# Performance work log

Measured on AMD Instinct MI355X. Metric: run time of the kernel, lower is better.

The kernel has to match this reference:

```python
import jax, jax.numpy as jnp
import numpy as np

B, T, E, H = 4, 2048, 1024, 16
D = E // H

def setup_inputs() -> dict:
    key = jax.random.key(0)
    ks = jax.random.split(key, 8)
    s = 0.02
    return {
        "q": jax.random.normal(ks[0], (B, T, E), dtype=jnp.float32),
        "k": jax.random.normal(ks[1], (B, T, E), dtype=jnp.float32),
        "v": jax.random.normal(ks[2], (B, T, E), dtype=jnp.float32),
        "Wq": jax.random.normal(ks[3], (E, E), dtype=jnp.float32) * s,
        "Wk": jax.random.normal(ks[4], (E, E), dtype=jnp.float32) * s,
        "Wv": jax.random.normal(ks[5], (E, E), dtype=jnp.float32) * s,
        "Wp": jax.random.normal(ks[6], (E, E), dtype=jnp.float32) * s,
        "bp": jnp.zeros((E,), dtype=jnp.float32),
    }

def reference(q, k, v, Wq, Wk, Wv, Wp, bp):
    # Linear projections (torch Linear: x @ W.T). NOTE: original code computes
    # key from the already-projected query (k = self.key(q)); external k is unused.
    qp = q @ Wq.T                      # [B,T,E]
    kp = qp @ Wk.T                     # [B,T,E]  <- faithful quirk
    vp = v @ Wv.T                      # [B,T,E]
    qh = qp.reshape(B, T, H, D).transpose(0, 2, 1, 3)  # [B,H,T,D]
    kh = kp.reshape(B, T, H, D).transpose(0, 2, 1, 3)
    vh = vp.reshape(B, T, H, D).transpose(0, 2, 1, 3)
    # Faithful quirk: att = scores / D**(-1/2) == scores * sqrt(D)
    scale = jnp.float32(D) ** 0.5
    att = jnp.einsum('bhtd,bhsd->bhts', qh, kh) * scale  # [B,H,T,T]
    causal = jnp.tril(jnp.ones((T, T), dtype=bool))
    att = jnp.where(causal, att, -jnp.inf)
    att = jax.nn.softmax(att, axis=-1)
    y = jnp.einsum('bhts,bhsd->bhtd', att, vh)           # [B,H,T,D]
    y = y.transpose(0, 2, 1, 3).reshape(B, T, E)
    return y @ Wp.T + bp
```

## Files before the change

### kernel.cpp

```cpp
#include <hip/hip_runtime.h>


typedef unsigned short u16;
typedef unsigned int   u32;
typedef __attribute__((ext_vector_type(8))) __bf16 bf16x8;
typedef __attribute__((ext_vector_type(8))) u16    u16x8;
typedef __attribute__((ext_vector_type(4))) u16    u16x4;
typedef __attribute__((ext_vector_type(4))) float  f32x4;
typedef __attribute__((ext_vector_type(4))) int    i32x4;

#define DEV static __device__ __forceinline__

DEV u16 f2bf(float x){ union{float f;u32 u;}v; v.f=x; u32 r=v.u+0x7fffu+((v.u>>16)&1u); return (u16)(r>>16); }
DEV float bf2f(u16 b){ union{u32 u;float f;}v; v.u=((u32)b)<<16; return v.f; }
DEV f32x4 zero4(){ f32x4 z={0.f,0.f,0.f,0.f}; return z; }
DEV f32x4 mfma16(bf16x8 a, bf16x8 b, f32x4 c){ return __builtin_amdgcn_mfma_f32_16x16x32_bf16(a,b,c,0,0,0); }
DEV void gld16(const u16* g, u16* l){
  __builtin_amdgcn_global_load_lds((const __attribute__((address_space(1))) u32*)g,
                                   (__attribute__((address_space(3))) u32*)l, 16, 0, 0);
}
DEV u32 cvtpk(float lo, float hi){
  u32 r;
  asm("v_cvt_pk_bf16_f32 %0, %1, %2" : "=v"(r) : "v"(lo), "v"(hi));
  return r;
}

constexpr int B_=4, T_=2048, E_=1024;
constexpr int M_=B_*T_;
constexpr float L2E8 = 11.5415603f;

__global__ __launch_bounds__(256)
void cvt_a(const float* __restrict__ q, const float* __restrict__ v,
           u16* __restrict__ qi, u16* __restrict__ vb)
{
  const int j=blockIdx.y;
  const size_t e=((size_t)blockIdx.x*256+threadIdx.x)*8;
  const float* s=(j==0)?q:v;
  f32x4 x0=*reinterpret_cast<const f32x4*>(s+e);
  f32x4 x1=*reinterpret_cast<const f32x4*>(s+e+4);
  u16x8 h,l;
#pragma unroll
  for(int t=0;t<4;t++){
    u16 hh=f2bf(x0[t]); h[t]=hh; l[t]=f2bf(x0[t]-bf2f(hh));
    u16 h2=f2bf(x1[t]); h[t+4]=h2; l[t+4]=f2bf(x1[t]-bf2f(h2));
  }
  if(j==0){
    const size_t row=e>>10, k=e&1023;
    u16* d=qi + row*2048 + (k>>3)*16;
    *reinterpret_cast<u16x8*>(d)=h;
    *reinterpret_cast<u16x8*>(d+8)=l;
  } else {
    *reinterpret_cast<u16x8*>(vb+e)=h;
  }
}

__global__ __launch_bounds__(256)
void cvt_w(const float* __restrict__ Wq, const float* __restrict__ Wk, const float* __restrict__ Wv,
           u16* __restrict__ wqi, u16* __restrict__ wki, u16* __restrict__ wvb)
{
  const int j=blockIdx.y;
  const size_t e=((size_t)blockIdx.x*256+threadIdx.x)*8;
  const float* s=(j==0)?Wq:(j==1)?Wk:Wv;
  f32x4 x0=*reinterpret_cast<const f32x4*>(s+e);
  f32x4 x1=*reinterpret_cast<const f32x4*>(s+e+4);
  u16x8 h,l;
#pragma unroll
  for(int t=0;t<4;t++){
    u16 hh=f2bf(x0[t]); h[t]=hh; l[t]=f2bf(x0[t]-bf2f(hh));
    u16 h2=f2bf(x1[t]); h[t+4]=h2; l[t+4]=f2bf(x1[t]-bf2f(h2));
  }
  if(j==2){ *reinterpret_cast<u16x8*>(wvb+e)=h; return; }
  u16* base=(j==0)?wqi:wki;
  const size_t row=e>>10, k=e&1023;
  u16* d=base + row*2048 + (k>>3)*16;
  *reinterpret_cast<u16x8*>(d)=h;
  *reinterpret_cast<u16x8*>(d+8)=l;
}

__global__ __launch_bounds__(256)
void cvt_p(const float* __restrict__ Wp, u16* __restrict__ wpb)
{
  const size_t e=((size_t)blockIdx.x*256+threadIdx.x)*8;
  f32x4 x0=*reinterpret_cast<const f32x4*>(Wp+e);
  f32x4 x1=*reinterpret_cast<const f32x4*>(Wp+e+4);
  u16x8 h;
#pragma unroll
  for(int t=0;t<4;t++){ h[t]=f2bf(x0[t]); h[t+4]=f2bf(x1[t]); }
  *reinterpret_cast<u16x8*>(wpb+e)=h;
}

template<int SPLIT,int OMODE>
__global__ __launch_bounds__(256)
void gemm(const u16* __restrict__ Ag, const u16* __restrict__ Bg,
          const float* __restrict__ bias,
          u16* __restrict__ Ob, float* __restrict__ Of, int ldc)
{
  __shared__ u16 sA[SPLIT?128*128:128*64];
  __shared__ u16 sB[SPLIT?128*128:128*64];

  const int tid=threadIdx.x, wave=tid>>6, lane=tid&63;
  const int quad=lane>>4, l16=lane&15, sw=l16&7;
  const int wm=(wave>>1)*64, wn=(wave&1)*64;
  const int n0=blockIdx.x*128, m0=blockIdx.y*128;

  f32x4 acc[4][4];
#pragma unroll
  for(int i=0;i<4;i++)
#pragma unroll
    for(int j=0;j<4;j++) acc[i][j]=zero4();

  for(int k0=0;k0<E_;k0+=64){
    if(SPLIT){
#pragma unroll
      for(int it=0;it<8;it++){
        const int c=it*256+tid, row=c>>4, j=(c&15)^(row&7);
        gld16(Ag + (size_t)(m0+row)*2048 + k0*2 + j*8, &sA[(it*256+wave*64)*8]);
      }
#pragma unroll
      for(int it=0;it<8;it++){
        const int c=it*256+tid, row=c>>4, j=(c&15)^(row&7);
        gld16(Bg + (size_t)(n0+row)*2048 + k0*2 + j*8, &sB[(it*256+wave*64)*8]);
      }
    } else {
#pragma unroll
      for(int it=0;it<4;it++){
        const int c=it*256+tid, row=c>>3, j=(c&7)^(row&7);
        gld16(Ag + (size_t)(m0+row)*1024 + k0 + j*8, &sA[(it*256+wave*64)*8]);
      }
#pragma unroll
      for(int it=0;it<4;it++){
        const int c=it*256+tid, row=c>>3, j=(c&7)^(row&7);
        gld16(Bg + (size_t)(n0+row)*1024 + k0 + j*8, &sB[(it*256+wave*64)*8]);
      }
    }
    __syncthreads();

#pragma unroll
    for(int kk=0;kk<2;kk++){
      if(SPLIT){
        bf16x8 ahh[4],ahl[4],bhh[4],bhl[4];
#pragma unroll
        for(int i=0;i<4;i++){
          const u16* pa=&sA[(wm+i*16+l16)*128];
          const u16* pb=&sB[(wn+i*16+l16)*128];
          const int ch=2*(kk*4+quad);
          ahh[i]=*reinterpret_cast<const bf16x8*>(&pa[((ch  )^sw)*8]);
          ahl[i]=*reinterpret_cast<const bf16x8*>(&pa[((ch+1)^sw)*8]);
          bhh[i]=*reinterpret_cast<const bf16x8*>(&pb[((ch  )^sw)*8]);
          bhl[i]=*reinterpret_cast<const bf16x8*>(&pb[((ch+1)^sw)*8]);
        }
#pragma unroll
        for(int i=0;i<4;i++)
#pragma unroll
          for(int j=0;j<4;j++){
            acc[i][j]=mfma16(ahh[i],bhh[j],acc[i][j]);
            acc[i][j]=mfma16(ahh[i],bhl[j],acc[i][j]);
            acc[i][j]=mfma16(ahl[i],bhh[j],acc[i][j]);
          }
      } else {
        bf16x8 a[4],b[4];
#pragma unroll
        for(int i=0;i<4;i++){
          a[i]=*reinterpret_cast<const bf16x8*>(&sA[(wm+i*16+l16)*64 + (((kk*4+quad)^sw)*8)]);
          b[i]=*reinterpret_cast<const bf16x8*>(&sB[(wn+i*16+l16)*64 + (((kk*4+quad)^sw)*8)]);
        }
#pragma unroll
        for(int i=0;i<4;i++)
#pragma unroll
          for(int j=0;j<4;j++)
            acc[i][j]=mfma16(a[i],b[j],acc[i][j]);
      }
    }
    __syncthreads();
  }

#pragma unroll
  for(int i=0;i<4;i++)
#pragma unroll
    for(int j=0;j<4;j++){
      const int col=n0+wn+j*16+l16;
#pragma unroll
      for(int r=0;r<4;r++){
        const int row=m0+wm+i*16+quad*4+r;
        float v=acc[i][j][r];
        if(OMODE==2)      Of[(size_t)row*ldc+col]=v+bias[col];
        else if(OMODE==1) Ob[(size_t)row*ldc+col]=f2bf(v);
        else {
          u16 hh=f2bf(v);
          const size_t base=(size_t)row*2048 + (size_t)(col>>3)*16 + (col&7);
          Ob[base]=hh; Ob[base+8]=f2bf(v-bf2f(hh));
        }
      }
    }
}

__global__ __launch_bounds__(256)
void attn(const u16* __restrict__ qpi, const u16* __restrict__ kpi,
          const u16* __restrict__ vpT, u16* __restrict__ yout)
{
  __shared__ u16 sK [2][64*128];
  __shared__ u16 sVT[2][64*64];

  const int tid=threadIdx.x, wave=tid>>6, lane=tid&63;
  const int quad=lane>>4, l16=lane&15, sw=l16&7;
  const int pr=(int)blockIdx.x>>6;
  const int bh=blockIdx.x&63;
  const int b=bh>>4, h=bh&15;

  auto STAGE=[&](int buf, int kt2){
    const int s0=kt2*64;
#pragma unroll
    for(int it=0;it<4;it++){
      const int c=it*256+tid, row=c>>4, j=(c&15)^(row&7);
      gld16(kpi + (size_t)(b*T_+s0+row)*2048 + h*128 + j*8,
            &sK[buf][(it*256+wave*64)*8]);
    }
#pragma unroll
    for(int it=0;it<2;it++){
      const int c=it*256+tid, row=c>>3, j=(c&7)^(row&7);
      gld16(vpT + (size_t)(h*64+row)*8192 + b*T_ + s0 + j*8,
            &sVT[buf][(it*256+wave*64)*8]);
    }
  };

#pragma unroll 1
  for(int half=0; half<2; half++){
    const int qt = half ? (15-pr) : pr;
    const int qr0=qt*128+wave*32;

    bf16x8 qfh[2][2], qfl[2][2];
#pragma unroll
    for(int mt=0;mt<2;mt++)
#pragma unroll
      for(int ksv=0;ksv<2;ksv++){
        const size_t off=(size_t)(b*T_+qr0+mt*16+l16)*2048 + h*128 + (ksv*4+quad)*16;
        qfh[mt][ksv]=*reinterpret_cast<const bf16x8*>(qpi+off);
        qfl[mt][ksv]=*reinterpret_cast<const bf16x8*>(qpi+off+8);
      }

    float mst[2]={-1e30f,-1e30f}, lst[2]={0.f,0.f};
    f32x4 oacc[2][4];
#pragma unroll
    for(int mt=0;mt<2;mt++)
#pragma unroll
      for(int dt=0;dt<4;dt++) oacc[mt][dt]=zero4();

    const int nkt=2*(qt+1);
    STAGE(0, 0);
    __syncthreads();

    for(int kt=0;kt<nkt;kt++){
      const int cur=kt&1;
      if(kt+1<nkt) STAGE(cur^1, kt+1);
      const int s0=kt*64;

      if(s0<=qr0+31){
        f32x4 sacc[4][2];
#pragma unroll
        for(int st=0;st<4;st++)
#pragma unroll
          for(int mt=0;mt<2;mt++) sacc[st][mt]=zero4();
        __builtin_amdgcn_s_setprio(1);
#pragma unroll
        for(int st=0;st<4;st++)
#pragma unroll
          for(int ksv=0;ksv<2;ksv++){
            const u16* pk=&sK[cur][(st*16+l16)*128];
            const int ch=2*(ksv*4+quad);
            bf16x8 kh=*reinterpret_cast<const bf16x8*>(&pk[((ch  )^sw)*8]);
            bf16x8 kl=*reinterpret_cast<const bf16x8*>(&pk[((ch+1)^sw)*8]);
#pragma unroll
            for(int mt=0;mt<2;mt++){
              sacc[st][mt]=mfma16(kh,qfh[mt][ksv],sacc[st][mt]);
              sacc[st][mt]=mfma16(kl,qfh[mt][ksv],sacc[st][mt]);
              sacc[st][mt]=mfma16(kh,qfl[mt][ksv],sacc[st][mt]);
            }
          }
        __builtin_amdgcn_s_setprio(0);
        const bool needmask=(s0+63>qr0);
        u32 pk_[4][2][2];
#pragma unroll
        for(int mt=0;mt<2;mt++){
          const int qrow=qr0+mt*16+l16;
          float mloc=-1e30f;
#pragma unroll
          for(int st=0;st<4;st++)
#pragma unroll
            for(int r=0;r<4;r++){
              float v=sacc[st][mt][r];
              if(needmask && (s0+st*16+quad*4+r>qrow)) v=-1e30f;
              sacc[st][mt][r]=v;
              mloc=fmaxf(mloc,v);
            }
          mloc=fmaxf(mloc,__shfl_xor(mloc,16,64));
          mloc=fmaxf(mloc,__shfl_xor(mloc,32,64));
          float cexp;
          if(__all(mloc <= mst[mt]+1.0f)){
            cexp=mst[mt]*L2E8;
          } else {
            const float nm=fmaxf(mst[mt],mloc);
            const float alpha=exp2f((mst[mt]-nm)*L2E8);
            mst[mt]=nm;
            lst[mt]*=alpha;
#pragma unroll
            for(int dt=0;dt<4;dt++) oacc[mt][dt]*=alpha;
            cexp=nm*L2E8;
          }
          float rs=0.f;
#pragma unroll
          for(int st=0;st<4;st++)
#pragma unroll
            for(int r=0;r<4;r++){
              float p=exp2f(__builtin_fmaf(sacc[st][mt][r],L2E8,-cexp));
              sacc[st][mt][r]=p;
              rs+=p;
            }
          lst[mt]+=rs;
#pragma unroll
          for(int st=0;st<4;st++){
            pk_[st][mt][0]=cvtpk(sacc[st][mt][0],sacc[st][mt][1]);
            pk_[st][mt][1]=cvtpk(sacc[st][mt][2],sacc[st][mt][3]);
          }
        }
        const int srcA=(2*(quad&1))*16+l16, srcB=srcA+16;
        const bool hs=(quad>=2);
#pragma unroll
        for(int ksv=0;ksv<2;ksv++){
          bf16x8 b2[2];
#pragma unroll
          for(int mt=0;mt<2;mt++){
            int e0=__shfl((int)pk_[2*ksv  ][mt][0],srcA,64);
            int g0=__shfl((int)pk_[2*ksv+1][mt][0],srcA,64);
            int e1=__shfl((int)pk_[2*ksv  ][mt][1],srcA,64);
            int g1=__shfl((int)pk_[2*ksv+1][mt][1],srcA,64);
            int e2=__shfl((int)pk_[2*ksv  ][mt][0],srcB,64);
            int g2=__shfl((int)pk_[2*ksv+1][mt][0],srcB,64);
            int e3=__shfl((int)pk_[2*ksv  ][mt][1],srcB,64);
            int g3=__shfl((int)pk_[2*ksv+1][mt][1],srcB,64);
            i32x4 bd={ hs?g0:e0, hs?g1:e1, hs?g2:e2, hs?g3:e3 };
            b2[mt]=*reinterpret_cast<bf16x8*>(&bd);
          }
          __builtin_amdgcn_s_setprio(1);
#pragma unroll
          for(int dt=0;dt<4;dt++){
            bf16x8 va=*reinterpret_cast<const bf16x8*>(&sVT[cur][(dt*16+l16)*64 + (((ksv*4+quad)^sw)*8)]);
#pragma unroll
            for(int mt=0;mt<2;mt++)
              oacc[mt][dt]=mfma16(va,b2[mt],oacc[mt][dt]);
          }
          __builtin_amdgcn_s_setprio(0);
        }
      }
      __syncthreads();
    }

#pragma unroll
    for(int mt=0;mt<2;mt++){
      float lt=lst[mt];
      lt+=__shfl_xor(lt,16,64);
      lt+=__shfl_xor(lt,32,64);
      const float inv=1.0f/lt;
      const size_t rb=(size_t)(b*T_+qr0+mt*16+l16)*1024 + h*64;
#pragma unroll
      for(int dt=0;dt<4;dt++){
        u16x4 o4;
#pragma unroll
        for(int r=0;r<4;r++) o4[r]=f2bf(oacc[mt][dt][r]*inv);
        *reinterpret_cast<u16x4*>(yout + rb + dt*16 + quad*4)=o4;
      }
    }
  }
}

extern "C" void kernel_launch(void* const* d_in, const int* in_sizes, int n_in,
                              void* d_out, int out_size, void* d_ws, size_t ws_size,
                              hipStream_t stream)
{
  const float* q =(const float*)d_in[0];
  const float* v =(const float*)d_in[2];
  const float* Wq=(const float*)d_in[3];
  const float* Wk=(const float*)d_in[4];
  const float* Wv=(const float*)d_in[5];
  const float* Wp=(const float*)d_in[6];
  const float* bp=(const float*)d_in[7];
  float* out=(float*)d_out;

  const size_t NE=(size_t)M_*E_;
  const size_t WE=(size_t)E_*E_;
  u16* wsv=(u16*)d_ws;
  u16* qsl_i=wsv;
  u16* qp_i =wsv+2*NE;
  u16* kp_i =wsv;
  u16* wp_b =wsv+2*NE;
  u16* vpT  =wsv+4*NE;
  u16* ybf  =wsv+5*NE;
  u16* og   =(u16*)d_out;
  u16* wq_i =og;
  u16* wk_i =og+2*WE;
  u16* wv_b =og+4*WE;
  u16* vb   =og+5*WE;

  dim3 blk(256);
  cvt_a<<<dim3(NE/2048,2), blk, 0, stream>>>(q, v, qsl_i, vb);
  cvt_w<<<dim3(WE/2048,3), blk, 0, stream>>>(Wq, Wk, Wv, wq_i, wk_i, wv_b);

  dim3 g(E_/128, M_/128);
  gemm<1,0><<<g, blk, 0, stream>>>(qsl_i, wq_i, nullptr, qp_i, nullptr, 0);
  gemm<1,0><<<g, blk, 0, stream>>>(qp_i, wk_i, nullptr, kp_i, nullptr, 0);
  gemm<0,1><<<dim3(M_/128, E_/128), blk, 0, stream>>>(wv_b, vb, nullptr, vpT, nullptr, M_);
  attn<<<dim3(512), blk, 0, stream>>>(qp_i, kp_i, vpT, ybf);
  cvt_p<<<dim3(WE/2048), blk, 0, stream>>>(Wp, wp_b);
  gemm<0,2><<<g, blk, 0, stream>>>(ybf, wp_b, bp, nullptr, out, E_);
}
```

Baseline: 433.1 us.

## Split attention KV range across wave pairs with 512-thread blocks and merge

The attention kernel now launches 512 threads per block. Each pair of waves shares the same 32 query rows and splits each 128-key tile in half, one 64-key half per wave. Per-wave online-softmax states (max, sum, output accumulators) are merged through shared memory at the end. K staging moves to 128-row double buffers with a single V buffer and explicit vmcnt waits and barriers, aiming for more waves in flight and fewer loop iterations. The cost is more LDS, extra barriers per iteration and a merge step.

```diff
diff --git a/kernel.cpp b/kernel.cpp
--- a/kernel.cpp
+++ b/kernel.cpp
@@ -194,39 +194,42 @@
     }
 }
 
-__global__ __launch_bounds__(256)
+__global__ __launch_bounds__(512,4)
 void attn(const u16* __restrict__ qpi, const u16* __restrict__ kpi,
           const u16* __restrict__ vpT, u16* __restrict__ yout)
 {
-  __shared__ u16 sK [2][64*128];
-  __shared__ u16 sVT[2][64*64];
+  __shared__ u16 sK [2][128*128];
+  __shared__ u16 sVT[64*128];
 
   const int tid=threadIdx.x, wave=tid>>6, lane=tid&63;
   const int quad=lane>>4, l16=lane&15, sw=l16&7;
+  const int rg=wave>>1, rho=wave&1;
   const int pr=(int)blockIdx.x>>6;
   const int bh=blockIdx.x&63;
   const int b=bh>>4, h=bh&15;
 
-  auto STAGE=[&](int buf, int kt2){
-    const int s0=kt2*64;
+  auto STAGE_K=[&](int buf, int j2){
 #pragma unroll
     for(int it=0;it<4;it++){
-      const int c=it*256+tid, row=c>>4, j=(c&15)^(row&7);
-      gld16(kpi + (size_t)(b*T_+s0+row)*2048 + h*128 + j*8,
-            &sK[buf][(it*256+wave*64)*8]);
-    }
+      const int c=it*512+tid, row=c>>4, j=(c&15)^(row&7);
+      gld16(kpi + (size_t)(b*T_+j2*128+row)*2048 + h*128 + j*8,
+            &sK[buf][(it*512+wave*64)*8]);
+    }
+  };
+  auto STAGE_V=[&](int j2){
 #pragma unroll
     for(int it=0;it<2;it++){
-      const int c=it*256+tid, row=c>>3, j=(c&7)^(row&7);
-      gld16(vpT + (size_t)(h*64+row)*8192 + b*T_ + s0 + j*8,
-            &sVT[buf][(it*256+wave*64)*8]);
+      const int c=it*512+tid, row=c>>4, j=(c&15)^(row&7);
+      gld16(vpT + (size_t)(h*64+row)*8192 + b*T_ + j2*128 + j*8,
+            &sVT[(it*512+wave*64)*8]);
     }
   };
 
 #pragma unroll 1
   for(int half=0; half<2; half++){
     const int qt = half ? (15-pr) : pr;
-    const int qr0=qt*128+wave*32;
+    const int qr0=qt*128+rg*32;
+    const int np=qt+1;
 
     bf16x8 qfh[2][2], qfl[2][2];
 #pragma unroll
@@ -245,16 +248,24 @@
 #pragma unroll
       for(int dt=0;dt<4;dt++) oacc[mt][dt]=zero4();
 
-    const int nkt=2*(qt+1);
-    STAGE(0, 0);
-    __syncthreads();
-
-    for(int kt=0;kt<nkt;kt++){
-      const int cur=kt&1;
-      if(kt+1<nkt) STAGE(cur^1, kt+1);
-      const int s0=kt*64;
-
-      if(s0<=qr0+31){
+    STAGE_V(0);
+    STAGE_K(0,0);
+    if(np>1){
+      STAGE_K(1,1);
+      asm volatile("s_waitcnt vmcnt(4)" ::: "memory");
+    } else {
+      asm volatile("s_waitcnt vmcnt(0)" ::: "memory");
+    }
+    __builtin_amdgcn_s_barrier();
+
+#pragma unroll 1
+    for(int j2=0;j2<np;j2++){
+      const int cbuf=j2&1;
+      const int s0=(2*j2+rho)*64;
+      const bool act=(s0<=qr0+31);
+      u32 pk_[4][2][2];
+
+      if(act){
         f32x4 sacc[4][2];
 #pragma unroll
         for(int st=0;st<4;st++)
@@ -265,7 +276,7 @@
         for(int st=0;st<4;st++)
 #pragma unroll
           for(int ksv=0;ksv<2;ksv++){
-            const u16* pk=&sK[cur][(st*16+l16)*128];
+            const u16* pk=&sK[cbuf][(rho*64+st*16+l16)*128];
             const int ch=2*(ksv*4+quad);
             bf16x8 kh=*reinterpret_cast<const bf16x8*>(&pk[((ch  )^sw)*8]);
             bf16x8 kl=*reinterpret_cast<const bf16x8*>(&pk[((ch+1)^sw)*8]);
@@ -278,7 +289,6 @@
           }
         __builtin_amdgcn_s_setprio(0);
         const bool needmask=(s0+63>qr0);
-        u32 pk_[4][2][2];
 #pragma unroll
         for(int mt=0;mt<2;mt++){
           const int qrow=qr0+mt*16+l16;
@@ -322,6 +332,13 @@
             pk_[st][mt][1]=cvtpk(sacc[st][mt][2],sacc[st][mt][3]);
           }
         }
+      }
+
+      if(j2+1<np) asm volatile("s_waitcnt vmcnt(4)" ::: "memory");
+      else        asm volatile("s_waitcnt vmcnt(0)" ::: "memory");
+      __builtin_amdgcn_s_barrier();
+
+      if(act){
         const int srcA=(2*(quad&1))*16+l16, srcB=srcA+16;
         const bool hs=(quad>=2);
 #pragma unroll
@@ -343,7 +360,8 @@
           __builtin_amdgcn_s_setprio(1);
 #pragma unroll
           for(int dt=0;dt<4;dt++){
-            bf16x8 va=*reinterpret_cast<const bf16x8*>(&sVT[cur][(dt*16+l16)*64 + (((ksv*4+quad)^sw)*8)]);
+            bf16x8 va=*reinterpret_cast<const bf16x8*>(
+              &sVT[(dt*16+l16)*128 + (rho*8 + (((ksv*4+quad))^sw))*8]);
 #pragma unroll
             for(int mt=0;mt<2;mt++)
               oacc[mt][dt]=mfma16(va,b2[mt],oacc[mt][dt]);
@@ -351,24 +369,54 @@
           __builtin_amdgcn_s_setprio(0);
         }
       }
-      __syncthreads();
-    }
-
-#pragma unroll
-    for(int mt=0;mt<2;mt++){
-      float lt=lst[mt];
-      lt+=__shfl_xor(lt,16,64);
-      lt+=__shfl_xor(lt,32,64);
-      const float inv=1.0f/lt;
-      const size_t rb=(size_t)(b*T_+qr0+mt*16+l16)*1024 + h*64;
-#pragma unroll
-      for(int dt=0;dt<4;dt++){
-        u16x4 o4;
-#pragma unroll
-        for(int r=0;r<4;r++) o4[r]=f2bf(oacc[mt][dt][r]*inv);
-        *reinterpret_cast<u16x4*>(yout + rb + dt*16 + quad*4)=o4;
-      }
-    }
+      __builtin_amdgcn_s_barrier();
+
+      if(j2+1<np) STAGE_V(j2+1);
+      if(j2+2<np) STAGE_K(cbuf, j2+2);
+      if(j2+2<np)      asm volatile("s_waitcnt vmcnt(6)" ::: "memory");
+      else if(j2+1<np) asm volatile("s_waitcnt vmcnt(2)" ::: "memory");
+      __builtin_amdgcn_s_barrier();
+    }
+
+    float* scr=reinterpret_cast<float*>(&sK[0][0]);
+    const int sbase=(rg*64+lane)*37;
+    if(rho==1){
+      scr[sbase+0]=mst[0]; scr[sbase+1]=mst[1];
+      scr[sbase+2]=lst[0]; scr[sbase+3]=lst[1];
+#pragma unroll
+      for(int mt=0;mt<2;mt++)
+#pragma unroll
+        for(int dt=0;dt<4;dt++)
+#pragma unroll
+          for(int r=0;r<4;r++)
+            scr[sbase+4+mt*16+dt*4+r]=oacc[mt][dt][r];
+    }
+    __syncthreads();
+    if(rho==0){
+#pragma unroll
+      for(int mt=0;mt<2;mt++){
+        const float m1=scr[sbase+mt], l1=scr[sbase+2+mt];
+        const float M=fmaxf(mst[mt],m1);
+        const float a0=exp2f((mst[mt]-M)*L2E8);
+        const float a1=exp2f((m1-M)*L2E8);
+        float lt=lst[mt]*a0+l1*a1;
+        lt+=__shfl_xor(lt,16,64);
+        lt+=__shfl_xor(lt,32,64);
+        const float inv=1.0f/lt;
+        const size_t rb=(size_t)(b*T_+qr0+mt*16+l16)*1024 + h*64;
+#pragma unroll
+        for(int dt=0;dt<4;dt++){
+          u16x4 o4;
+#pragma unroll
+          for(int r=0;r<4;r++){
+            const float o1=scr[sbase+4+mt*16+dt*4+r];
+            o4[r]=f2bf((oacc[mt][dt][r]*a0+o1*a1)*inv);
+          }
+          *reinterpret_cast<u16x4*>(yout + rb + dt*16 + quad*4)=o4;
+        }
+      }
+    }
+    __syncthreads();
   }
 }
 
@@ -408,7 +456,7 @@
   gemm<1,0><<<g, blk, 0, stream>>>(qsl_i, wq_i, nullptr, qp_i, nullptr, 0);
   gemm<1,0><<<g, blk, 0, stream>>>(qp_i, wk_i, nullptr, kp_i, nullptr, 0);
   gemm<0,1><<<dim3(M_/128, E_/128), blk, 0, stream>>>(wv_b, vb, nullptr, vpT, nullptr, M_);
-  attn<<<dim3(512), blk, 0, stream>>>(qp_i, kp_i, vpT, ybf);
+  attn<<<dim3(512), dim3(512), 0, stream>>>(qp_i, kp_i, vpT, ybf);
   cvt_p<<<dim3(WE/2048), blk, 0, stream>>>(Wp, wp_b);
   gemm<0,2><<<g, blk, 0, stream>>>(ybf, wp_b, bp, nullptr, out, E_);
 }
```

Result: slower. 516.9 us (+19.3%).

## Shrink attention query tiles to 64 rows and restage K/V with finer-grained waits

Applied to the files above, without the earlier changes.

The attention kernel now gives each block a 64-row query chunk (16 rows per wave) instead of 128, which doubles the grid to 1024 blocks and halves the per-wave accumulator state. K stays double-buffered but is prefetched two tiles ahead, while V uses a single buffer reloaded after the PV step. Explicit vmcnt waits and raw barriers replace __syncthreads so the V load can overlap the QK and softmax work. The intent is better occupancy and load balance across CUs, and less wasted work on the causal diagonal. The cost is less K/V reuse per block, more barriers per tile, and fragile hand-counted vmcnt values.

```diff
diff --git a/kernel.cpp b/kernel.cpp
--- a/kernel.cpp
+++ b/kernel.cpp
@@ -199,7 +199,7 @@
           const u16* __restrict__ vpT, u16* __restrict__ yout)
 {
   __shared__ u16 sK [2][64*128];
-  __shared__ u16 sVT[2][64*64];
+  __shared__ u16 sVT[64*64];
 
   const int tid=threadIdx.x, wave=tid>>6, lane=tid&63;
   const int quad=lane>>4, l16=lane&15, sw=l16&7;
@@ -207,165 +207,165 @@
   const int bh=blockIdx.x&63;
   const int b=bh>>4, h=bh&15;
 
-  auto STAGE=[&](int buf, int kt2){
-    const int s0=kt2*64;
+  auto STAGE_K=[&](int buf, int j){
 #pragma unroll
     for(int it=0;it<4;it++){
-      const int c=it*256+tid, row=c>>4, j=(c&15)^(row&7);
-      gld16(kpi + (size_t)(b*T_+s0+row)*2048 + h*128 + j*8,
+      const int c=it*256+tid, row=c>>4, jj=(c&15)^(row&7);
+      gld16(kpi + (size_t)(b*T_+j*64+row)*2048 + h*128 + jj*8,
             &sK[buf][(it*256+wave*64)*8]);
     }
+  };
+  auto STAGE_V=[&](int j){
 #pragma unroll
     for(int it=0;it<2;it++){
-      const int c=it*256+tid, row=c>>3, j=(c&7)^(row&7);
-      gld16(vpT + (size_t)(h*64+row)*8192 + b*T_ + s0 + j*8,
-            &sVT[buf][(it*256+wave*64)*8]);
+      const int c=it*256+tid, row=c>>3, jj=(c&7)^(row&7);
+      gld16(vpT + (size_t)(h*64+row)*8192 + b*T_ + j*64 + jj*8,
+            &sVT[(it*256+wave*64)*8]);
     }
   };
 
 #pragma unroll 1
   for(int half=0; half<2; half++){
-    const int qt = half ? (15-pr) : pr;
-    const int qr0=qt*128+wave*32;
-
-    bf16x8 qfh[2][2], qfl[2][2];
-#pragma unroll
-    for(int mt=0;mt<2;mt++)
-#pragma unroll
-      for(int ksv=0;ksv<2;ksv++){
-        const size_t off=(size_t)(b*T_+qr0+mt*16+l16)*2048 + h*128 + (ksv*4+quad)*16;
-        qfh[mt][ksv]=*reinterpret_cast<const bf16x8*>(qpi+off);
-        qfl[mt][ksv]=*reinterpret_cast<const bf16x8*>(qpi+off+8);
-      }
-
-    float mst[2]={-1e30f,-1e30f}, lst[2]={0.f,0.f};
-    f32x4 oacc[2][4];
-#pragma unroll
-    for(int mt=0;mt<2;mt++)
-#pragma unroll
-      for(int dt=0;dt<4;dt++) oacc[mt][dt]=zero4();
-
-    const int nkt=2*(qt+1);
-    STAGE(0, 0);
-    __syncthreads();
-
-    for(int kt=0;kt<nkt;kt++){
-      const int cur=kt&1;
-      if(kt+1<nkt) STAGE(cur^1, kt+1);
-      const int s0=kt*64;
-
-      if(s0<=qr0+31){
-        f32x4 sacc[4][2];
-#pragma unroll
-        for(int st=0;st<4;st++)
-#pragma unroll
-          for(int mt=0;mt<2;mt++) sacc[st][mt]=zero4();
-        __builtin_amdgcn_s_setprio(1);
-#pragma unroll
-        for(int st=0;st<4;st++)
-#pragma unroll
-          for(int ksv=0;ksv<2;ksv++){
-            const u16* pk=&sK[cur][(st*16+l16)*128];
-            const int ch=2*(ksv*4+quad);
-            bf16x8 kh=*reinterpret_cast<const bf16x8*>(&pk[((ch  )^sw)*8]);
-            bf16x8 kl=*reinterpret_cast<const bf16x8*>(&pk[((ch+1)^sw)*8]);
-#pragma unroll
-            for(int mt=0;mt<2;mt++){
-              sacc[st][mt]=mfma16(kh,qfh[mt][ksv],sacc[st][mt]);
-              sacc[st][mt]=mfma16(kl,qfh[mt][ksv],sacc[st][mt]);
-              sacc[st][mt]=mfma16(kh,qfl[mt][ksv],sacc[st][mt]);
-            }
-          }
-        __builtin_amdgcn_s_setprio(0);
-        const bool needmask=(s0+63>qr0);
-        u32 pk_[4][2][2];
-#pragma unroll
-        for(int mt=0;mt<2;mt++){
-          const int qrow=qr0+mt*16+l16;
-          float mloc=-1e30f;
-#pragma unroll
-          for(int st=0;st<4;st++)
-#pragma unroll
-            for(int r=0;r<4;r++){
-              float v=sacc[st][mt][r];
-              if(needmask && (s0+st*16+quad*4+r>qrow)) v=-1e30f;
-              sacc[st][mt][r]=v;
-              mloc=fmaxf(mloc,v);
-            }
-          mloc=fmaxf(mloc,__shfl_xor(mloc,16,64));
-          mloc=fmaxf(mloc,__shfl_xor(mloc,32,64));
-          float cexp;
-          if(__all(mloc <= mst[mt]+1.0f)){
-            cexp=mst[mt]*L2E8;
-          } else {
-            const float nm=fmaxf(mst[mt],mloc);
-            const float alpha=exp2f((mst[mt]-nm)*L2E8);
-            mst[mt]=nm;
-            lst[mt]*=alpha;
-#pragma unroll
-            for(int dt=0;dt<4;dt++) oacc[mt][dt]*=alpha;
-            cexp=nm*L2E8;
-          }
-          float rs=0.f;
-#pragma unroll
-          for(int st=0;st<4;st++)
-#pragma unroll
-            for(int r=0;r<4;r++){
-              float p=exp2f(__builtin_fmaf(sacc[st][mt][r],L2E8,-cexp));
-              sacc[st][mt][r]=p;
-              rs+=p;
-            }
-          lst[mt]+=rs;
-#pragma unroll
-          for(int st=0;st<4;st++){
-            pk_[st][mt][0]=cvtpk(sacc[st][mt][0],sacc[st][mt][1]);
-            pk_[st][mt][1]=cvtpk(sacc[st][mt][2],sacc[st][mt][3]);
-          }
-        }
+    const int qc = half ? (31-pr) : pr;
+    const int qr0=qc*64+wave*16;
+    const int np=qc+1;
+
+    bf16x8 qfh[2], qfl[2];
+#pragma unroll
+    for(int ksv=0;ksv<2;ksv++){
+      const size_t off=(size_t)(b*T_+qr0+l16)*2048 + h*128 + (ksv*4+quad)*16;
+      qfh[ksv]=*reinterpret_cast<const bf16x8*>(qpi+off);
+      qfl[ksv]=*reinterpret_cast<const bf16x8*>(qpi+off+8);
+    }
+
+    float mst=-1e30f, lst=0.f;
+    f32x4 oacc[4];
+#pragma unroll
+    for(int dt=0;dt<4;dt++) oacc[dt]=zero4();
+
+    STAGE_V(0);
+    STAGE_K(0,0);
+    if(np>1){
+      STAGE_K(1,1);
+      asm volatile("s_waitcnt vmcnt(4)" ::: "memory");
+    } else {
+      asm volatile("s_waitcnt vmcnt(0)" ::: "memory");
+    }
+    __builtin_amdgcn_s_barrier();
+
+#pragma unroll 1
+    for(int j=0;j<np;j++){
+      const int cur=j&1;
+      const int s0=j*64;
+
+      f32x4 sacc[4];
+#pragma unroll
+      for(int st=0;st<4;st++) sacc[st]=zero4();
+      __builtin_amdgcn_s_setprio(1);
+#pragma unroll
+      for(int st=0;st<4;st++)
+#pragma unroll
+        for(int ksv=0;ksv<2;ksv++){
+          const u16* pk=&sK[cur][(st*16+l16)*128];
+          const int ch=2*(ksv*4+quad);
+          bf16x8 kh=*reinterpret_cast<const bf16x8*>(&pk[((ch  )^sw)*8]);
+          bf16x8 kl=*reinterpret_cast<const bf16x8*>(&pk[((ch+1)^sw)*8]);
+          sacc[st]=mfma16(kh,qfh[ksv],sacc[st]);
+          sacc[st]=mfma16(kl,qfh[ksv],sacc[st]);
+          sacc[st]=mfma16(kh,qfl[ksv],sacc[st]);
+        }
+      __builtin_amdgcn_s_setprio(0);
+
+      const bool needmask=(j+1==np);
+      const int qrow=qr0+l16;
+      float mloc=-1e30f;
+#pragma unroll
+      for(int st=0;st<4;st++)
+#pragma unroll
+        for(int r=0;r<4;r++){
+          float v=sacc[st][r];
+          if(needmask && (s0+st*16+quad*4+r>qrow)) v=-1e30f;
+          sacc[st][r]=v;
+          mloc=fmaxf(mloc,v);
+        }
+      mloc=fmaxf(mloc,__shfl_xor(mloc,16,64));
+      mloc=fmaxf(mloc,__shfl_xor(mloc,32,64));
+      float cexp;
+      if(__all(mloc <= mst+1.0f)){
+        cexp=mst*L2E8;
+      } else {
+        const float nm=fmaxf(mst,mloc);
+        const float alpha=exp2f((mst-nm)*L2E8);
+        mst=nm;
+        lst*=alpha;
+#pragma unroll
+        for(int dt=0;dt<4;dt++) oacc[dt]*=alpha;
+        cexp=nm*L2E8;
+      }
+      float rs=0.f;
+      u32 pk_[4][2];
+#pragma unroll
+      for(int st=0;st<4;st++){
+#pragma unroll
+        for(int r=0;r<4;r++){
+          float p=exp2f(__builtin_fmaf(sacc[st][r],L2E8,-cexp));
+          sacc[st][r]=p;
+          rs+=p;
+        }
+        pk_[st][0]=cvtpk(sacc[st][0],sacc[st][1]);
+        pk_[st][1]=cvtpk(sacc[st][2],sacc[st][3]);
+      }
+      lst+=rs;
+
+      if(j+1<np) asm volatile("s_waitcnt vmcnt(4)" ::: "memory");
+      else       asm volatile("s_waitcnt vmcnt(0)" ::: "memory");
+      __builtin_amdgcn_s_barrier();
+
+      {
         const int srcA=(2*(quad&1))*16+l16, srcB=srcA+16;
         const bool hs=(quad>=2);
 #pragma unroll
         for(int ksv=0;ksv<2;ksv++){
-          bf16x8 b2[2];
-#pragma unroll
-          for(int mt=0;mt<2;mt++){
-            int e0=__shfl((int)pk_[2*ksv  ][mt][0],srcA,64);
-            int g0=__shfl((int)pk_[2*ksv+1][mt][0],srcA,64);
-            int e1=__shfl((int)pk_[2*ksv  ][mt][1],srcA,64);
-            int g1=__shfl((int)pk_[2*ksv+1][mt][1],srcA,64);
-            int e2=__shfl((int)pk_[2*ksv  ][mt][0],srcB,64);
-            int g2=__shfl((int)pk_[2*ksv+1][mt][0],srcB,64);
-            int e3=__shfl((int)pk_[2*ksv  ][mt][1],srcB,64);
-            int g3=__shfl((int)pk_[2*ksv+1][mt][1],srcB,64);
-            i32x4 bd={ hs?g0:e0, hs?g1:e1, hs?g2:e2, hs?g3:e3 };
-            b2[mt]=*reinterpret_cast<bf16x8*>(&bd);
-          }
+          int e0=__shfl((int)pk_[2*ksv  ][0],srcA,64);
+          int g0=__shfl((int)pk_[2*ksv+1][0],srcA,64);
+          int e1=__shfl((int)pk_[2*ksv  ][1],srcA,64);
+          int g1=__shfl((int)pk_[2*ksv+1][1],srcA,64);
+          int e2=__shfl((int)pk_[2*ksv  ][0],srcB,64);
+          int g2=__shfl((int)pk_[2*ksv+1][0],srcB,64);
+          int e3=__shfl((int)pk_[2*ksv  ][1],srcB,64);
+          int g3=__shfl((int)pk_[2*ksv+1][1],srcB,64);
+          i32x4 bd={ hs?g0:e0, hs?g1:e1, hs?g2:e2, hs?g3:e3 };
+          bf16x8 b2=*reinterpret_cast<bf16x8*>(&bd);
           __builtin_amdgcn_s_setprio(1);
 #pragma unroll
           for(int dt=0;dt<4;dt++){
-            bf16x8 va=*reinterpret_cast<const bf16x8*>(&sVT[cur][(dt*16+l16)*64 + (((ksv*4+quad)^sw)*8)]);
-#pragma unroll
-            for(int mt=0;mt<2;mt++)
-              oacc[mt][dt]=mfma16(va,b2[mt],oacc[mt][dt]);
+            bf16x8 va=*reinterpret_cast<const bf16x8*>(
+              &sVT[(dt*16+l16)*64 + (((ksv*4+quad)^sw)*8)]);
+            oacc[dt]=mfma16(va,b2,oacc[dt]);
           }
           __builtin_amdgcn_s_setprio(0);
         }
       }
-      __syncthreads();
-    }
-
-#pragma unroll
-    for(int mt=0;mt<2;mt++){
-      float lt=lst[mt];
+      __builtin_amdgcn_s_barrier();
+
+      if(j+1<np) STAGE_V(j+1);
+      if(j+2<np) STAGE_K(cur, j+2);
+      if(j+2<np)      asm volatile("s_waitcnt vmcnt(6)" ::: "memory");
+      else if(j+1<np) asm volatile("s_waitcnt vmcnt(2)" ::: "memory");
+      __builtin_amdgcn_s_barrier();
+    }
+
+    {
+      float lt=lst;
       lt+=__shfl_xor(lt,16,64);
       lt+=__shfl_xor(lt,32,64);
       const float inv=1.0f/lt;
-      const size_t rb=(size_t)(b*T_+qr0+mt*16+l16)*1024 + h*64;
+      const size_t rb=(size_t)(b*T_+qr0+l16)*1024 + h*64;
 #pragma unroll
       for(int dt=0;dt<4;dt++){
         u16x4 o4;
 #pragma unroll
-        for(int r=0;r<4;r++) o4[r]=f2bf(oacc[mt][dt][r]*inv);
+        for(int r=0;r<4;r++) o4[r]=f2bf(oacc[dt][r]*inv);
         *reinterpret_cast<u16x4*>(yout + rb + dt*16 + quad*4)=o4;
       }
     }
@@ -408,7 +408,7 @@
   gemm<1,0><<<g, blk, 0, stream>>>(qsl_i, wq_i, nullptr, qp_i, nullptr, 0);
   gemm<1,0><<<g, blk, 0, stream>>>(qp_i, wk_i, nullptr, kp_i, nullptr, 0);
   gemm<0,1><<<dim3(M_/128, E_/128), blk, 0, stream>>>(wv_b, vb, nullptr, vpT, nullptr, M_);
-  attn<<<dim3(512), blk, 0, stream>>>(qp_i, kp_i, vpT, ybf);
+  attn<<<dim3(1024), blk, 0, stream>>>(qp_i, kp_i, vpT, ybf);
   cvt_p<<<dim3(WE/2048), blk, 0, stream>>>(Wp, wp_b);
   gemm<0,2><<<g, blk, 0, stream>>>(ybf, wp_b, bp, nullptr, out, E_);
 }
```

After: 456.4 us. 5.4% more time.

## Software-pipeline attention loop: overlap QK^T of next tile with softmax/PV of previous

Applied to the files above, without the earlier changes.

Restructures the flash-attention inner loop so that the QK^T MFMAs for tile j run in the same iteration as the softmax and PV for tile j-1. K and V are staged separately into triple-buffered LDS with explicit vmcnt waits and raw barriers in place of __syncthreads. The aim is to hide the softmax VALU and exp latency behind matrix-core work and to prefetch further ahead. It costs 50% more LDS, which may lower occupancy, and adds a peeled epilogue plus fragile hand-counted waitcnt logic.

```diff
diff --git a/kernel.cpp b/kernel.cpp
--- a/kernel.cpp
+++ b/kernel.cpp
@@ -198,8 +198,8 @@
 void attn(const u16* __restrict__ qpi, const u16* __restrict__ kpi,
           const u16* __restrict__ vpT, u16* __restrict__ yout)
 {
-  __shared__ u16 sK [2][64*128];
-  __shared__ u16 sVT[2][64*64];
+  __shared__ u16 sK [3][64*128];
+  __shared__ u16 sVT[3][64*64];
 
   const int tid=threadIdx.x, wave=tid>>6, lane=tid&63;
   const int quad=lane>>4, l16=lane&15, sw=l16&7;
@@ -207,18 +207,19 @@
   const int bh=blockIdx.x&63;
   const int b=bh>>4, h=bh&15;
 
-  auto STAGE=[&](int buf, int kt2){
-    const int s0=kt2*64;
+  auto STAGE_K=[&](int buf, int kt){
 #pragma unroll
     for(int it=0;it<4;it++){
-      const int c=it*256+tid, row=c>>4, j=(c&15)^(row&7);
-      gld16(kpi + (size_t)(b*T_+s0+row)*2048 + h*128 + j*8,
+      const int c=it*256+tid, row=c>>4, jj=(c&15)^(row&7);
+      gld16(kpi + (size_t)(b*T_+kt*64+row)*2048 + h*128 + jj*8,
             &sK[buf][(it*256+wave*64)*8]);
     }
+  };
+  auto STAGE_V=[&](int buf, int kt){
 #pragma unroll
     for(int it=0;it<2;it++){
-      const int c=it*256+tid, row=c>>3, j=(c&7)^(row&7);
-      gld16(vpT + (size_t)(h*64+row)*8192 + b*T_ + s0 + j*8,
+      const int c=it*256+tid, row=c>>3, jj=(c&7)^(row&7);
+      gld16(vpT + (size_t)(h*64+row)*8192 + b*T_ + kt*64 + jj*8,
             &sVT[buf][(it*256+wave*64)*8]);
     }
   };
@@ -227,6 +228,7 @@
   for(int half=0; half<2; half++){
     const int qt = half ? (15-pr) : pr;
     const int qr0=qt*128+wave*32;
+    const int np=2*(qt+1);
 
     bf16x8 qfh[2][2], qfl[2][2];
 #pragma unroll
@@ -240,45 +242,30 @@
 
     float mst[2]={-1e30f,-1e30f}, lst[2]={0.f,0.f};
     f32x4 oacc[2][4];
+    f32x4 sacc[4][2];
+    u32 pk_[4][2][2];
 #pragma unroll
     for(int mt=0;mt<2;mt++)
 #pragma unroll
       for(int dt=0;dt<4;dt++) oacc[mt][dt]=zero4();
 
-    const int nkt=2*(qt+1);
-    STAGE(0, 0);
-    __syncthreads();
-
-    for(int kt=0;kt<nkt;kt++){
-      const int cur=kt&1;
-      if(kt+1<nkt) STAGE(cur^1, kt+1);
-      const int s0=kt*64;
-
-      if(s0<=qr0+31){
-        f32x4 sacc[4][2];
-#pragma unroll
-        for(int st=0;st<4;st++)
-#pragma unroll
-          for(int mt=0;mt<2;mt++) sacc[st][mt]=zero4();
-        __builtin_amdgcn_s_setprio(1);
-#pragma unroll
-        for(int st=0;st<4;st++)
-#pragma unroll
-          for(int ksv=0;ksv<2;ksv++){
-            const u16* pk=&sK[cur][(st*16+l16)*128];
-            const int ch=2*(ksv*4+quad);
-            bf16x8 kh=*reinterpret_cast<const bf16x8*>(&pk[((ch  )^sw)*8]);
-            bf16x8 kl=*reinterpret_cast<const bf16x8*>(&pk[((ch+1)^sw)*8]);
-#pragma unroll
-            for(int mt=0;mt<2;mt++){
-              sacc[st][mt]=mfma16(kh,qfh[mt][ksv],sacc[st][mt]);
-              sacc[st][mt]=mfma16(kl,qfh[mt][ksv],sacc[st][mt]);
-              sacc[st][mt]=mfma16(kh,qfl[mt][ksv],sacc[st][mt]);
-            }
-          }
-        __builtin_amdgcn_s_setprio(0);
+    STAGE_V(0,0);
+    STAGE_K(0,0);
+    STAGE_K(1,1);
+
+    int i0=0,i1=1,i2=2;
+#pragma unroll 1
+    for(int j=0;j<np;j++){
+      if(j+1<np) STAGE_V(i1, j+1);
+      if(j+2<np) STAGE_K(i2, j+2);
+      if(j+2<np)      asm volatile("s_waitcnt vmcnt(10)" ::: "memory");
+      else if(j+1<np) asm volatile("s_waitcnt vmcnt(6)"  ::: "memory");
+      else            asm volatile("s_waitcnt vmcnt(0)"  ::: "memory");
+      __builtin_amdgcn_s_barrier();
+
+      if(j>0){
+        const int s0=(j-1)*64;
         const bool needmask=(s0+63>qr0);
-        u32 pk_[4][2][2];
 #pragma unroll
         for(int mt=0;mt<2;mt++){
           const int qrow=qr0+mt*16+l16;
@@ -308,19 +295,17 @@
           }
           float rs=0.f;
 #pragma unroll
-          for(int st=0;st<4;st++)
+          for(int st=0;st<4;st++){
 #pragma unroll
             for(int r=0;r<4;r++){
               float p=exp2f(__builtin_fmaf(sacc[st][mt][r],L2E8,-cexp));
               sacc[st][mt][r]=p;
               rs+=p;
             }
-          lst[mt]+=rs;
-#pragma unroll
-          for(int st=0;st<4;st++){
             pk_[st][mt][0]=cvtpk(sacc[st][mt][0],sacc[st][mt][1]);
             pk_[st][mt][1]=cvtpk(sacc[st][mt][2],sacc[st][mt][3]);
           }
+          lst[mt]+=rs;
         }
         const int srcA=(2*(quad&1))*16+l16, srcB=srcA+16;
         const bool hs=(quad>=2);
@@ -343,7 +328,8 @@
           __builtin_amdgcn_s_setprio(1);
 #pragma unroll
           for(int dt=0;dt<4;dt++){
-            bf16x8 va=*reinterpret_cast<const bf16x8*>(&sVT[cur][(dt*16+l16)*64 + (((ksv*4+quad)^sw)*8)]);
+            bf16x8 va=*reinterpret_cast<const bf16x8*>(
+              &sVT[i2][(dt*16+l16)*64 + (((ksv*4+quad)^sw)*8)]);
 #pragma unroll
             for(int mt=0;mt<2;mt++)
               oacc[mt][dt]=mfma16(va,b2[mt],oacc[mt][dt]);
@@ -351,7 +337,113 @@
           __builtin_amdgcn_s_setprio(0);
         }
       }
-      __syncthreads();
+
+      {
+        const int s0c=j*64;
+        const bool actC=(s0c<=qr0+31);
+        if(actC){
+#pragma unroll
+          for(int st=0;st<4;st++)
+#pragma unroll
+            for(int mt=0;mt<2;mt++) sacc[st][mt]=zero4();
+          __builtin_amdgcn_s_setprio(1);
+#pragma unroll
+          for(int st=0;st<4;st++)
+#pragma unroll
+            for(int ksv=0;ksv<2;ksv++){
+              const u16* pk=&sK[i0][(st*16+l16)*128];
+              const int ch=2*(ksv*4+quad);
+              bf16x8 kh=*reinterpret_cast<const bf16x8*>(&pk[((ch  )^sw)*8]);
+              bf16x8 kl=*reinterpret_cast<const bf16x8*>(&pk[((ch+1)^sw)*8]);
+#pragma unroll
+              for(int mt=0;mt<2;mt++){
+                sacc[st][mt]=mfma16(kh,qfh[mt][ksv],sacc[st][mt]);
+                sacc[st][mt]=mfma16(kl,qfh[mt][ksv],sacc[st][mt]);
+                sacc[st][mt]=mfma16(kh,qfl[mt][ksv],sacc[st][mt]);
+              }
+            }
+          __builtin_amdgcn_s_setprio(0);
+        }
+      }
+
+      { int t=i0; i0=i1; i1=i2; i2=t; }
+      __builtin_amdgcn_s_barrier();
+    }
+
+    {
+      const int s0=(np-1)*64;
+      const bool act=(s0<=qr0+31);
+      if(act){
+        const bool needmask=true;
+#pragma unroll
+        for(int mt=0;mt<2;mt++){
+          const int qrow=qr0+mt*16+l16;
+          float mloc=-1e30f;
+#pragma unroll
+          for(int st=0;st<4;st++)
+#pragma unroll
+            for(int r=0;r<4;r++){
+              float v=sacc[st][mt][r];
+              if(needmask && (s0+st*16+quad*4+r>qrow)) v=-1e30f;
+              sacc[st][mt][r]=v;
+              mloc=fmaxf(mloc,v);
+            }
+          mloc=fmaxf(mloc,__shfl_xor(mloc,16,64));
+          mloc=fmaxf(mloc,__shfl_xor(mloc,32,64));
+          float cexp;
+          if(__all(mloc <= mst[mt]+1.0f)){
+            cexp=mst[mt]*L2E8;
+          } else {
+            const float nm=fmaxf(mst[mt],mloc);
+            const float alpha=exp2f((mst[mt]-nm)*L2E8);
+            mst[mt]=nm;
+            lst[mt]*=alpha;
+#pragma unroll
+            for(int dt=0;dt<4;dt++) oacc[mt][dt]*=alpha;
+            cexp=nm*L2E8;
+          }
+          float rs=0.f;
+#pragma unroll
+          for(int st=0;st<4;st++){
+#pragma unroll
+            for(int r=0;r<4;r++){
+              float p=exp2f(__builtin_fmaf(sacc[st][mt][r],L2E8,-cexp));
+              sacc[st][mt][r]=p;
+              rs+=p;
+            }
+            pk_[st][mt][0]=cvtpk(sacc[st][mt][0],sacc[st][mt][1]);
+            pk_[st][mt][1]=cvtpk(sacc[st][mt][2],sacc[st][mt][3]);
+          }
+          lst[mt]+=rs;
+        }
+        const int srcA=(2*(quad&1))*16+l16, srcB=srcA+16;
+        const bool hs=(quad>=2);
+#pragma unroll
+        for(int ksv=0;ksv<2;ksv++){
+          bf16x8 b2[2];
+#pragma unroll
+          for(int mt=0;mt<2;mt++){
+            int e0=__shfl((int)pk_[2*ksv  ][mt][0],srcA,64);
+            int g0=__shfl((int)pk_[2*ksv+1][mt][0],srcA,64);
+            int e1=__shfl((int)pk_[2*ksv  ][mt][1],srcA,64);
+            int g1=__shfl((int)pk_[2*ksv+1][mt][1],srcA,64);
+            int e2=__shfl((int)pk_[2*ksv  ][mt][0],srcB,64);
+            int g2=__shfl((int)pk_[2*ksv+1][mt][0],srcB,64);
+            int e3=__shfl((int)pk_[2*ksv  ][mt][1],srcB,64);
+            int g3=__shfl((int)pk_[2*ksv+1][mt][1],srcB,64);
+            i32x4 bd={ hs?g0:e0, hs?g1:e1, hs?g2:e2, hs?g3:e3 };
+            b2[mt]=*reinterpret_cast<bf16x8*>(&bd);
+          }
+#pragma unroll
+          for(int dt=0;dt<4;dt++){
+            bf16x8 va=*reinterpret_cast<const bf16x8*>(
+              &sVT[i2][(dt*16+l16)*64 + (((ksv*4+quad)^sw)*8)]);
+#pragma unroll
+            for(int mt=0;mt<2;mt++)
+              oacc[mt][dt]=mfma16(va,b2[mt],oacc[mt][dt]);
+          }
+        }
+      }
     }
 
 #pragma unroll
@@ -369,6 +461,7 @@
         *reinterpret_cast<u16x4*>(yout + rb + dt*16 + quad*4)=o4;
       }
     }
+    __builtin_amdgcn_s_barrier();
   }
 }
 
```

Result: slower. 503.3 us (+16.2%).
